# Kernel tuning notes

Measured on AMD Instinct MI355X. Metric: run time of the kernel, lower is better.

Reference implementation:

```python
import jax, jax.numpy as jnp
import numpy as np

LIDAR_MAX_X = 32.0
LIDAR_MAX_Y = 32.0


def bilinear_grid_sample(value, grid):
    """torch.nn.functional.grid_sample, mode='bilinear', padding_mode='zeros',
    align_corners=False.
    value: (B, C, H, W); grid: (B, Q, P, 2) in [-1, 1] (x=width, y=height).
    Returns (B, C, Q, P)."""
    B, C, H, W = value.shape
    x = (grid[..., 0] + 1.0) * (W / 2) - 0.5  # (B,Q,P) unnormalized col
    y = (grid[..., 1] + 1.0) * (H / 2) - 0.5  # (B,Q,P) unnormalized row
    x0 = jnp.floor(x)
    y0 = jnp.floor(y)
    x1 = x0 + 1.0
    y1 = y0 + 1.0
    wx1 = x - x0
    wx0 = 1.0 - wx1
    wy1 = y - y0
    wy0 = 1.0 - wy1
    vflat = value.reshape(B, C, H * W)

    def gather(ix, iy):
        valid = (ix >= 0) & (ix <= W - 1) & (iy >= 0) & (iy <= H - 1)
        ixc = jnp.clip(ix, 0, W - 1).astype(jnp.int32)
        iyc = jnp.clip(iy, 0, H - 1).astype(jnp.int32)
        idx = iyc * W + ixc  # (B,Q,P)
        g = jax.vmap(lambda v, i: v[:, i])(vflat, idx)  # (B,C,Q,P)
        return g * valid[:, None, :, :].astype(value.dtype)

    out = (gather(x0, y0) * (wx0 * wy0)[:, None]
           + gather(x1, y0) * (wx1 * wy0)[:, None]
           + gather(x0, y1) * (wx0 * wy1)[:, None]
           + gather(x1, y1) * (wx1 * wy1)[:, None])
    return out


def setup_inputs() -> dict:
    key = jax.random.key(0)
    ks = jax.random.split(key, 10)
    bs, Q, P, D = 16, 1024, 8, 256
    Cin, H, W = 64, 128, 128
    queries = jax.random.normal(ks[0], (bs, Q, D), dtype=jnp.float32)
    # scale so trajectory points span the +/-32m BEV extent
    traj_points = jax.random.normal(ks[1], (bs, Q, P, 2), dtype=jnp.float32) * 20.0
    bev_feature = jax.random.normal(ks[2], (bs, Cin, H, W), dtype=jnp.float32)
    spatial_shape = jnp.array([H, W], dtype=jnp.int64)
    attn_w = jax.random.normal(ks[3], (P, D), dtype=jnp.float32) * 0.02
    attn_b = jnp.zeros((P,), dtype=jnp.float32)
    conv_w = jax.random.normal(ks[4], (256, Cin, 3, 3), dtype=jnp.float32) * 0.05
    conv_b = jnp.zeros((256,), dtype=jnp.float32)
    out_w = jax.random.normal(ks[5], (D, D), dtype=jnp.float32) * (1.0 / np.sqrt(D))
    out_b = jnp.zeros((D,), dtype=jnp.float32)
    return {"queries": queries, "traj_points": traj_points,
            "bev_feature": bev_feature, "spatial_shape": spatial_shape,
            "attn_w": attn_w, "attn_b": attn_b,
            "conv_w": conv_w, "conv_b": conv_b,
            "out_w": out_w, "out_b": out_b}


def reference(queries, traj_points, bev_feature, spatial_shape,
              attn_w, attn_b, conv_w, conv_b, out_w, out_b):
    # normalize trajectory to [-1,1] and swap (y,x) -> (x,y) grid order
    grid = jnp.stack([traj_points[..., 1] / LIDAR_MAX_X,
                      traj_points[..., 0] / LIDAR_MAX_Y], axis=-1)  # (bs,Q,P,2)
    # per-query attention over the P sampled points
    attn = jax.nn.softmax(
        jnp.einsum('bqd,pd->bqp', queries, attn_w) + attn_b, axis=-1)  # (bs,Q,P)
    # value projection: 3x3 conv + ReLU
    value = jax.lax.conv_general_dilated(
        bev_feature, conv_w, window_strides=(1, 1),
        padding=((1, 1), (1, 1)),
        dimension_numbers=('NCHW', 'OIHW', 'NCHW'))
    value = jax.nn.relu(value + conv_b[None, :, None, None])  # (bs,256,H,W)
    sampled = bilinear_grid_sample(value, grid)  # (bs,256,Q,P)
    out = jnp.einsum('bcqp,bqp->bqc', sampled, attn)  # weighted sum + permute
    out = jnp.einsum('bqc,dc->bqd', out, out_w) + out_b
    # dropout is identity in eval mode
    return out + queries
```

## Files before the change

kernel.cpp:

```cpp
#include <hip/hip_runtime.h>
#include <stdint.h>


typedef __attribute__((ext_vector_type(8))) short short8;
typedef __attribute__((ext_vector_type(4))) float f32x4;

__device__ __forceinline__ unsigned short f2bf(float f) {
  union { float f; unsigned int u; } v; v.f = f;
  unsigned int r = (v.u + 0x7FFFu + ((v.u >> 16) & 1u)) >> 16;
  return (unsigned short)r;
}
__device__ __forceinline__ float bf2f(unsigned short h) {
  union { unsigned int u; float f; } v; v.u = ((unsigned int)h) << 16;
  return v.f;
}

__device__ __forceinline__ void gload_lds16(const void* g, void* l) {
  __builtin_amdgcn_global_load_lds(
      (const __attribute__((address_space(1))) unsigned int*)g,
      (__attribute__((address_space(3))) unsigned int*)l, 16, 0, 0);
}

__global__ __launch_bounds__(256) void k1_transpose(const float* __restrict__ bev,
                                                    unsigned short* __restrict__ nhwc) {
  __shared__ __align__(16) float lds[64 * 32 * 4];
  const int b = blockIdx.x >> 7, y = blockIdx.x & 127;
  const int t = threadIdx.x;
  const float* src = bev + (size_t)(b * 64) * 16384 + y * 128;
#pragma unroll
  for (int k = 0; k < 8; ++k) {
    int chunk = k * 256 + t;
    int ic = chunk >> 5, xq = chunk & 31;
    float4 v = *(const float4*)(src + ic * 16384 + xq * 4);
    int slot = xq ^ (ic >> 3);
    *(float4*)&lds[(ic * 32 + slot) * 4] = v;
  }
  __syncthreads();
  unsigned short* dst = nhwc + (size_t)blockIdx.x * 8192;
#pragma unroll
  for (int k = 0; k < 4; ++k) {
    int co = k * 256 + t;
    int x = co >> 3, icg = co & 7;
    int slot = (x >> 2) ^ icg;
    int w = x & 3;
    uint4 u;
    unsigned int* up = (unsigned int*)&u;
#pragma unroll
    for (int jj = 0; jj < 4; ++jj) {
      float v0 = lds[((icg * 8 + 2 * jj) * 32 + slot) * 4 + w];
      float v1 = lds[((icg * 8 + 2 * jj + 1) * 32 + slot) * 4 + w];
      up[jj] = (unsigned int)f2bf(v0) | ((unsigned int)f2bf(v1) << 16);
    }
    *(uint4*)(dst + x * 64 + icg * 8) = u;
  }
}

__global__ __launch_bounds__(256) void k1b_pack(const float* __restrict__ conv_w,
                                                const float* __restrict__ out_w,
                                                unsigned short* __restrict__ wconv,
                                                unsigned short* __restrict__ wout,
                                                float* __restrict__ zp) {
  const int tid = blockIdx.x * 256 + threadIdx.x;
  for (int idx = tid; idx < 9 * 8 * 256 * 8; idx += 16384) {
    int j = idx & 7, oc = (idx >> 3) & 255, g = (idx >> 11) & 7, o = idx >> 14;
    wconv[idx] = f2bf(conv_w[(oc * 64 + g * 8 + j) * 9 + o]);
  }
  for (int idx = tid; idx < 32 * 256 * 8; idx += 16384) {
    int j = idx & 7, d = (idx >> 3) & 255, g = idx >> 11;
    wout[idx] = f2bf(out_w[d * 256 + g * 8 + j]);
  }
  if (tid < 64) zp[tid] = 0.0f;
}

#define K2_WOFF 66560
__global__ __launch_bounds__(512, 2) void k2_conv(const unsigned short* __restrict__ nhwc,
                                                  const unsigned short* __restrict__ wconv,
                                                  const float* __restrict__ conv_b,
                                                  const float* __restrict__ zp,
                                                  unsigned short* __restrict__ value) {
  __shared__ __align__(16) char smem[99328];
  const short8* lin = (const short8*)smem;
  const int bid = blockIdx.x;
  const int swz = (bid & 7) * 128 + (bid >> 3);
  const int b = swz >> 6, yp = swz & 63;
  const int y0 = yp * 2;
  const int t = threadIdx.x, wid = t >> 6, lane = t & 63;
  const int wo = wid >> 2, wp = wid & 3;
  const int g = lane >> 4, l15 = lane & 15;
  const int r_hat = wp >> 1;
  const int xbase = (wp & 1) * 64 + l15;

  const unsigned short* bevb = nhwc + (size_t)b * (128 * 128 * 64);
  for (int i = wid; i < 65; i += 8) {
    const int chunk = i * 64 + lane;
    const int ridx = chunk / 1040;
    const int rem = chunk - ridx * 1040;
    const int icg = rem / 130;
    const int c = rem - icg * 130;
    const int yy = y0 - 1 + ridx, xx = c - 1;
    const void* src = (yy >= 0 && yy < 128 && xx >= 0 && xx < 128)
                          ? (const void*)(bevb + ((yy * 128 + xx) * 64 + icg * 8))
                          : (const void*)zp;
    gload_lds16(src, smem + i * 1024);
  }
  {
    const unsigned short* wsrc = wconv;
    gload_lds16(wsrc + (size_t)(wid * 128 + lane) * 8, smem + K2_WOFF + wid * 2048);
    gload_lds16(wsrc + (size_t)(wid * 128 + 64 + lane) * 8, smem + K2_WOFF + wid * 2048 + 1024);
  }
  __syncthreads();

  const f32x4 z4 = {0.f, 0.f, 0.f, 0.f};
  f32x4 acc[8][4];
#pragma unroll
  for (int i = 0; i < 8; ++i)
#pragma unroll
    for (int j = 0; j < 4; ++j) acc[i][j] = z4;

#pragma unroll
  for (int s = 0; s < 18; ++s) {
    const int o = s >> 1, ich = s & 1;
    const int dyr = o / 3;
    const int dx = o - dyr * 3 - 1;
    if (s < 17) {
      const int s1 = s + 1;
      const unsigned short* wsrc = wconv + (size_t)(((s1 >> 1) * 2048 + (s1 & 1) * 1024)) * 8;
      char* wdst = smem + K2_WOFF + ((s1 & 1) ? 16384 : 0) + wid * 2048;
      gload_lds16(wsrc + (size_t)(wid * 128 + lane) * 8, wdst);
      gload_lds16(wsrc + (size_t)(wid * 128 + 64 + lane) * 8, wdst + 1024);
    }
    const short8* wb = (const short8*)(smem + K2_WOFF + ((s & 1) ? 16384 : 0));
    short8 af[8];
#pragma unroll
    for (int ocf = 0; ocf < 8; ++ocf) af[ocf] = wb[g * 256 + wo * 128 + ocf * 16 + l15];
    short8 bf[4];
    const int cb = ((r_hat + dyr) * 8 + ich * 4 + g) * 130 + xbase + 1 + dx;
#pragma unroll
    for (int pf = 0; pf < 4; ++pf) bf[pf] = lin[cb + pf * 16];
    __builtin_amdgcn_s_setprio(1);
#pragma unroll
    for (int ocf = 0; ocf < 8; ++ocf)
#pragma unroll
      for (int pf = 0; pf < 4; ++pf)
        acc[ocf][pf] = __builtin_amdgcn_mfma_f32_16x16x32_bf16(af[ocf], bf[pf], acc[ocf][pf], 0, 0, 0);
    __builtin_amdgcn_s_setprio(0);
    __syncthreads();
  }

  const int y = y0 + r_hat;
  unsigned short* vrow = value + (((size_t)(b * 128 + y) * 128 + xbase) * 256);
#pragma unroll
  for (int ocf = 0; ocf < 8; ++ocf) {
    const int ocb = wo * 128 + ocf * 16 + g * 4;
    const float4 cb4 = *(const float4*)(conv_b + ocb);
#pragma unroll
    for (int pf = 0; pf < 4; ++pf) {
      ushort4 ov;
      float v0 = acc[ocf][pf][0] + cb4.x; ov.x = f2bf(v0 > 0.f ? v0 : 0.f);
      float v1 = acc[ocf][pf][1] + cb4.y; ov.y = f2bf(v1 > 0.f ? v1 : 0.f);
      float v2 = acc[ocf][pf][2] + cb4.z; ov.z = f2bf(v2 > 0.f ? v2 : 0.f);
      float v3 = acc[ocf][pf][3] + cb4.w; ov.w = f2bf(v3 > 0.f ? v3 : 0.f);
      *(ushort4*)(vrow + (size_t)pf * 16 * 256 + ocb) = ov;
    }
  }
}

__global__ __launch_bounds__(256) void k3_sample(const float* __restrict__ queries,
                                                 const float* __restrict__ traj,
                                                 const float* __restrict__ attn_w,
                                                 const float* __restrict__ attn_b,
                                                 const unsigned short* __restrict__ value,
                                                 unsigned short* __restrict__ S) {
  const int wid = threadIdx.x >> 6, lane = threadIdx.x & 63;
  const int qg = blockIdx.x * 4 + wid;
  const int b = qg >> 10;
  const float4 qv = ((const float4*)queries)[qg * 64 + lane];
  float a[8];
#pragma unroll
  for (int p = 0; p < 8; ++p) {
    float4 wv = ((const float4*)attn_w)[p * 64 + lane];
    float d = qv.x * wv.x + qv.y * wv.y + qv.z * wv.z + qv.w * wv.w;
#pragma unroll
    for (int off = 32; off >= 1; off >>= 1) d += __shfl_xor(d, off);
    a[p] = d + attn_b[p];
  }
  float mx = a[0];
#pragma unroll
  for (int p = 1; p < 8; ++p) mx = fmaxf(mx, a[p]);
  float ssum = 0.f;
#pragma unroll
  for (int p = 0; p < 8; ++p) { a[p] = __expf(a[p] - mx); ssum += a[p]; }
  const float inv = 1.f / ssum;

  float acc0 = 0.f, acc1 = 0.f, acc2 = 0.f, acc3 = 0.f;
  const unsigned short* vb = value + (size_t)b * (128 * 128 * 256);
  const int coff = lane * 4;
#pragma unroll
  for (int p = 0; p < 8; ++p) {
    const float ty = traj[(qg * 8 + p) * 2 + 0];
    const float tx = traj[(qg * 8 + p) * 2 + 1];
    const float fx = (tx * 0.03125f + 1.f) * 64.f - 0.5f;
    const float fy = (ty * 0.03125f + 1.f) * 64.f - 0.5f;
    const float fx0 = floorf(fx), fy0 = floorf(fy);
    const int ix0 = (int)fx0, iy0 = (int)fy0;
    const float wx1 = fx - fx0, wx0 = 1.f - wx1;
    const float wy1 = fy - fy0, wy0 = 1.f - wy1;
    const float ap = a[p] * inv;
    const float cw[4] = {wx0 * wy0 * ap, wx1 * wy0 * ap, wx0 * wy1 * ap, wx1 * wy1 * ap};
    const int cx[4] = {ix0, ix0 + 1, ix0, ix0 + 1};
    const int cy[4] = {iy0, iy0, iy0 + 1, iy0 + 1};
#pragma unroll
    for (int cc = 0; cc < 4; ++cc) {
      if (cx[cc] >= 0 && cx[cc] < 128 && cy[cc] >= 0 && cy[cc] < 128) {
        const ushort4 v = *(const ushort4*)(vb + (cy[cc] * 128 + cx[cc]) * 256 + coff);
        acc0 += cw[cc] * bf2f(v.x);
        acc1 += cw[cc] * bf2f(v.y);
        acc2 += cw[cc] * bf2f(v.z);
        acc3 += cw[cc] * bf2f(v.w);
      }
    }
  }
  ushort4 o;
  o.x = f2bf(acc0); o.y = f2bf(acc1); o.z = f2bf(acc2); o.w = f2bf(acc3);
  *(ushort4*)(S + (size_t)qg * 256 + coff) = o;
}

__global__ __launch_bounds__(256, 2) void k4_proj(const unsigned short* __restrict__ S,
                                                  const unsigned short* __restrict__ wout,
                                                  const float* __restrict__ out_b,
                                                  const float* __restrict__ queries,
                                                  float* __restrict__ out) {
  __shared__ __align__(16) char smem[16384];
  const short8* lds8 = (const short8*)smem;
  const short8* wp8 = (const short8*)wout;
  const int t = threadIdx.x, wid = t >> 6, lane = t & 63;
  const int wo = wid >> 1, wq = wid & 1;
  const int q0 = blockIdx.x * 128;
  const int g = lane >> 4, l15 = lane & 15;
  const f32x4 z4 = {0.f, 0.f, 0.f, 0.f};
  f32x4 acc[8][4];
#pragma unroll
  for (int i = 0; i < 8; ++i)
#pragma unroll
    for (int j = 0; j < 4; ++j) acc[i][j] = z4;

#pragma unroll
  for (int ii = 0; ii < 2; ++ii) {
    const int chunk = wid * 128 + ii * 64 + lane;
    const int gg = chunk >> 7, q = chunk & 127;
    gload_lds16(S + ((size_t)(q0 + q) * 256 + gg * 8), smem + wid * 2048 + ii * 1024);
  }
  __syncthreads();

#pragma unroll
  for (int ks = 0; ks < 8; ++ks) {
    if (ks < 7) {
      const int k1 = ks + 1;
#pragma unroll
      for (int ii = 0; ii < 2; ++ii) {
        const int chunk = wid * 128 + ii * 64 + lane;
        const int gg = chunk >> 7, q = chunk & 127;
        gload_lds16(S + ((size_t)(q0 + q) * 256 + k1 * 32 + gg * 8),
                    smem + ((k1 & 1) ? 8192 : 0) + wid * 2048 + ii * 1024);
      }
    }
    short8 af[8];
#pragma unroll
    for (int df = 0; df < 8; ++df)
      af[df] = wp8[(ks * 4 + g) * 256 + wo * 128 + df * 16 + l15];
    short8 bf[4];
    const short8* sb = lds8 + ((ks & 1) ? 512 : 0);
#pragma unroll
    for (int qf = 0; qf < 4; ++qf) bf[qf] = sb[g * 128 + wq * 64 + qf * 16 + l15];
    __builtin_amdgcn_s_setprio(1);
#pragma unroll
    for (int df = 0; df < 8; ++df)
#pragma unroll
      for (int qf = 0; qf < 4; ++qf)
        acc[df][qf] = __builtin_amdgcn_mfma_f32_16x16x32_bf16(af[df], bf[qf], acc[df][qf], 0, 0, 0);
    __builtin_amdgcn_s_setprio(0);
    __syncthreads();
  }

#pragma unroll
  for (int df = 0; df < 8; ++df) {
    const int db = wo * 128 + df * 16 + g * 4;
    const float4 ob4 = *(const float4*)(out_b + db);
#pragma unroll
    for (int qf = 0; qf < 4; ++qf) {
      const int q = q0 + wq * 64 + qf * 16 + l15;
      const float4 qv = *(const float4*)(queries + (size_t)q * 256 + db);
      float4 ov;
      ov.x = acc[df][qf][0] + ob4.x + qv.x;
      ov.y = acc[df][qf][1] + ob4.y + qv.y;
      ov.z = acc[df][qf][2] + ob4.z + qv.z;
      ov.w = acc[df][qf][3] + ob4.w + qv.w;
      *(float4*)(out + (size_t)q * 256 + db) = ov;
    }
  }
}

extern "C" void kernel_launch(void* const* d_in, const int* in_sizes, int n_in,
                              void* d_out, int out_size, void* d_ws, size_t ws_size,
                              hipStream_t stream) {
  const float* queries = (const float*)d_in[0];
  const float* traj    = (const float*)d_in[1];
  const float* bev     = (const float*)d_in[2];
  const float* attn_w  = (const float*)d_in[4];
  const float* attn_b  = (const float*)d_in[5];
  const float* conv_w  = (const float*)d_in[6];
  const float* conv_b  = (const float*)d_in[7];
  const float* out_w   = (const float*)d_in[8];
  const float* out_b   = (const float*)d_in[9];
  float* out = (float*)d_out;

  char* ws = (char*)d_ws;
  unsigned short* bev_nhwc = (unsigned short*)(ws);
  unsigned short* value    = (unsigned short*)(ws + 33554432);
  unsigned short* wconv    = (unsigned short*)(ws + 167772160);
  unsigned short* wout     = (unsigned short*)(ws + 168067072);
  unsigned short* Sbuf     = (unsigned short*)(ws + 168198144);
  float*          zp       = (float*)(ws + 176586752);

  k1_transpose<<<2048, 256, 0, stream>>>(bev, bev_nhwc);
  k1b_pack<<<64, 256, 0, stream>>>(conv_w, out_w, wconv, wout, zp);
  k2_conv<<<1024, 512, 0, stream>>>(bev_nhwc, wconv, conv_b, zp, value);
  k3_sample<<<4096, 256, 0, stream>>>(queries, traj, attn_w, attn_b, value, Sbuf);
  k4_proj<<<128, 256, 0, stream>>>(Sbuf, wout, out_b, queries, out);
}
```

Before: 173.8 us.

## Restructure conv main loop into phased ping-pong schedule with per-tap weight staging

The conv kernel now stages the weights for a whole 3x3 tap (both input-channel halves) per iteration into a larger double-buffered LDS region, where before it staged half a tap per step. Each tap is split into four MFMA phases separated by raw s_barriers, with LDS fragment reads and global-to-LDS weight loads interleaved between phases so memory traffic overlaps with matrix math. LDS use grows from about 97KB to 129KB per block. With launch bounds of two blocks per CU this may reduce occupancy, and the many extra barriers add synchronisation cost.

```diff
diff --git a/kernel.cpp b/kernel.cpp
--- a/kernel.cpp
+++ b/kernel.cpp
@@ -73,12 +73,53 @@
 }
 
 #define K2_WOFF 66560
+
+#define K2_READA(o, h) do {                                                   \
+    const short8* wb_ = (const short8*)(smem + K2_WOFF + ((o)&1) * 32768);    \
+    _Pragma("unroll")                                                         \
+    for (int ic_ = 0; ic_ < 2; ++ic_)                                         \
+      _Pragma("unroll")                                                       \
+      for (int i_ = 0; i_ < 4; ++i_)                                          \
+        aH[ic_*4+i_] = wb_[(ic_*4+g)*256 + wo*128 + (h)*64 + i_*16 + l15];    \
+  } while (0)
+
+#define K2_READB(dyr, dx, j, B) do {                                          \
+    _Pragma("unroll")                                                         \
+    for (int ic_ = 0; ic_ < 2; ++ic_)                                         \
+      _Pragma("unroll")                                                       \
+      for (int p_ = 0; p_ < 2; ++p_)                                          \
+        B[ic_*2+p_] = lin[((rh+(dyr))*8 + ic_*4 + g)*130 + 1 + (dx) + xb +    \
+                          l15 + ((j)*2 + p_)*16];                             \
+  } while (0)
+
+#define K2_STAGEW(o1, cbase) do {                                             \
+    const unsigned short* ws_ = wconv + (size_t)(o1) * 16384;                 \
+    char* wd_ = smem + K2_WOFF + ((o1)&1) * 32768;                            \
+    _Pragma("unroll")                                                         \
+    for (int c_ = 0; c_ < 4; ++c_)                                            \
+      gload_lds16(ws_ + ((cbase)+c_) * 512 + lane * 8,                        \
+                  wd_ + ((cbase)+c_) * 1024);                                 \
+  } while (0)
+
+#define K2_MF(h, j, B) do {                                                   \
+    __builtin_amdgcn_s_setprio(1);                                            \
+    _Pragma("unroll")                                                         \
+    for (int i_ = 0; i_ < 4; ++i_)                                            \
+      _Pragma("unroll")                                                       \
+      for (int p_ = 0; p_ < 2; ++p_)                                          \
+        _Pragma("unroll")                                                     \
+        for (int ic_ = 0; ic_ < 2; ++ic_)                                     \
+          acc[(h)*4+i_][(j)*2+p_] = __builtin_amdgcn_mfma_f32_16x16x32_bf16(  \
+              aH[ic_*4+i_], B[ic_*2+p_], acc[(h)*4+i_][(j)*2+p_], 0, 0, 0);   \
+    __builtin_amdgcn_s_setprio(0);                                            \
+  } while (0)
+
 __global__ __launch_bounds__(512, 2) void k2_conv(const unsigned short* __restrict__ nhwc,
                                                   const unsigned short* __restrict__ wconv,
                                                   const float* __restrict__ conv_b,
                                                   const float* __restrict__ zp,
                                                   unsigned short* __restrict__ value) {
-  __shared__ __align__(16) char smem[99328];
+  __shared__ __align__(16) char smem[132096];
   const short8* lin = (const short8*)smem;
   const int bid = blockIdx.x;
   const int swz = (bid & 7) * 128 + (bid >> 3);
@@ -87,8 +128,8 @@
   const int t = threadIdx.x, wid = t >> 6, lane = t & 63;
   const int wo = wid >> 2, wp = wid & 3;
   const int g = lane >> 4, l15 = lane & 15;
-  const int r_hat = wp >> 1;
-  const int xbase = (wp & 1) * 64 + l15;
+  const int rh = wp >> 1;
+  const int xb = (wp & 1) * 64;
 
   const unsigned short* bevb = nhwc + (size_t)b * (128 * 128 * 64);
   for (int i = wid; i < 65; i += 8) {
@@ -103,12 +144,9 @@
                           : (const void*)zp;
     gload_lds16(src, smem + i * 1024);
   }
-  {
-    const unsigned short* wsrc = wconv;
-    gload_lds16(wsrc + (size_t)(wid * 128 + lane) * 8, smem + K2_WOFF + wid * 2048);
-    gload_lds16(wsrc + (size_t)(wid * 128 + 64 + lane) * 8, smem + K2_WOFF + wid * 2048 + 1024);
-  }
-  __syncthreads();
+  K2_STAGEW(0, wid * 4);
+  asm volatile("s_waitcnt vmcnt(0)" ::: "memory");
+  __builtin_amdgcn_s_barrier();
 
   const f32x4 z4 = {0.f, 0.f, 0.f, 0.f};
   f32x4 acc[8][4];
@@ -117,38 +155,34 @@
 #pragma unroll
     for (int j = 0; j < 4; ++j) acc[i][j] = z4;
 
-#pragma unroll
-  for (int s = 0; s < 18; ++s) {
-    const int o = s >> 1, ich = s & 1;
-    const int dyr = o / 3;
-    const int dx = o - dyr * 3 - 1;
-    if (s < 17) {
-      const int s1 = s + 1;
-      const unsigned short* wsrc = wconv + (size_t)(((s1 >> 1) * 2048 + (s1 & 1) * 1024)) * 8;
-      char* wdst = smem + K2_WOFF + ((s1 & 1) ? 16384 : 0) + wid * 2048;
-      gload_lds16(wsrc + (size_t)(wid * 128 + lane) * 8, wdst);
-      gload_lds16(wsrc + (size_t)(wid * 128 + 64 + lane) * 8, wdst + 1024);
-    }
-    const short8* wb = (const short8*)(smem + K2_WOFF + ((s & 1) ? 16384 : 0));
-    short8 af[8];
-#pragma unroll
-    for (int ocf = 0; ocf < 8; ++ocf) af[ocf] = wb[g * 256 + wo * 128 + ocf * 16 + l15];
-    short8 bf[4];
-    const int cb = ((r_hat + dyr) * 8 + ich * 4 + g) * 130 + xbase + 1 + dx;
-#pragma unroll
-    for (int pf = 0; pf < 4; ++pf) bf[pf] = lin[cb + pf * 16];
-    __builtin_amdgcn_s_setprio(1);
-#pragma unroll
-    for (int ocf = 0; ocf < 8; ++ocf)
-#pragma unroll
-      for (int pf = 0; pf < 4; ++pf)
-        acc[ocf][pf] = __builtin_amdgcn_mfma_f32_16x16x32_bf16(af[ocf], bf[pf], acc[ocf][pf], 0, 0, 0);
-    __builtin_amdgcn_s_setprio(0);
-    __syncthreads();
-  }
-
-  const int y = y0 + r_hat;
-  unsigned short* vrow = value + (((size_t)(b * 128 + y) * 128 + xbase) * 256);
+  short8 aH[8], b0[4], b1[4];
+
+#pragma unroll
+  for (int o = 0; o < 9; ++o) {
+    const int dyr = o / 3, dx = o % 3 - 1;
+    K2_READA(o, 0);
+    K2_READB(dyr, dx, 0, b0);
+    if (o < 8 && wid < 4) K2_STAGEW(o + 1, wid * 4);
+    __builtin_amdgcn_s_barrier();
+    K2_MF(0, 0, b0);
+    __builtin_amdgcn_s_barrier();
+    K2_READB(dyr, dx, 1, b1);
+    if (o < 8 && wid >= 4) K2_STAGEW(o + 1, 16 + (wid - 4) * 4);
+    __builtin_amdgcn_s_barrier();
+    K2_MF(0, 1, b1);
+    __builtin_amdgcn_s_barrier();
+    K2_READA(o, 1);
+    __builtin_amdgcn_s_barrier();
+    K2_MF(1, 0, b0);
+    __builtin_amdgcn_s_barrier();
+    asm volatile("s_waitcnt vmcnt(0)" ::: "memory");
+    __builtin_amdgcn_s_barrier();
+    K2_MF(1, 1, b1);
+    __builtin_amdgcn_s_barrier();
+  }
+
+  const int y = y0 + rh;
+  unsigned short* vrow = value + (((size_t)(b * 128 + y) * 128 + xb + l15) * 256);
 #pragma unroll
   for (int ocf = 0; ocf < 8; ++ocf) {
     const int ocb = wo * 128 + ocf * 16 + g * 4;
```

Result: slower. 182.3 us (+4.9%).

## Load conv weights directly to registers with double-buffered prefetch, drop per-step barriers

Applied to the files above, without the earlier changes.

The conv kernel no longer stages weight slices through shared memory. Each wave now loads its A fragments straight from global memory into registers two steps ahead, and prefetches the B fragments from LDS one step ahead. Dropping the weight staging removes the per-step __syncthreads and cuts LDS use from about 97KB to 65KB, which could allow more blocks per CU. The cost is more VGPR pressure from the double-buffered fragments, and every wave issues its own uncoalesced global weight loads, which rely on cache hits.

```diff
diff --git a/kernel.cpp b/kernel.cpp
--- a/kernel.cpp
+++ b/kernel.cpp
@@ -72,14 +72,40 @@
   if (tid < 64) zp[tid] = 0.0f;
 }
 
-#define K2_WOFF 66560
+#define K2_LOADA(s, A) do {                                                   \
+    _Pragma("unroll")                                                         \
+    for (int ocf_ = 0; ocf_ < 8; ++ocf_)                                      \
+      A[ocf_] = gA[(4 * (s) + g) * 256 + wo * 128 + ocf_ * 16 + l15];         \
+  } while (0)
+
+#define K2_READB(s, B) do {                                                   \
+    const int o_ = (s) >> 1, ich_ = (s) & 1;                                  \
+    const int dyr_ = o_ / 3, dx_ = o_ - dyr_ * 3 - 1;                         \
+    _Pragma("unroll")                                                         \
+    for (int pf_ = 0; pf_ < 4; ++pf_)                                         \
+      B[pf_] = lin[((rh + dyr_) * 8 + ich_ * 4 + g) * 130 + 1 + dx_ + xb +    \
+                   l15 + pf_ * 16];                                           \
+  } while (0)
+
+#define K2_MFMA(A, B) do {                                                    \
+    __builtin_amdgcn_s_setprio(1);                                            \
+    _Pragma("unroll")                                                         \
+    for (int ocf_ = 0; ocf_ < 8; ++ocf_)                                      \
+      _Pragma("unroll")                                                       \
+      for (int pf_ = 0; pf_ < 4; ++pf_)                                       \
+        acc[ocf_][pf_] = __builtin_amdgcn_mfma_f32_16x16x32_bf16(             \
+            A[ocf_], B[pf_], acc[ocf_][pf_], 0, 0, 0);                        \
+    __builtin_amdgcn_s_setprio(0);                                            \
+  } while (0)
+
 __global__ __launch_bounds__(512, 2) void k2_conv(const unsigned short* __restrict__ nhwc,
                                                   const unsigned short* __restrict__ wconv,
                                                   const float* __restrict__ conv_b,
                                                   const float* __restrict__ zp,
                                                   unsigned short* __restrict__ value) {
-  __shared__ __align__(16) char smem[99328];
+  __shared__ __align__(16) char smem[66560];
   const short8* lin = (const short8*)smem;
+  const short8* gA = (const short8*)wconv;
   const int bid = blockIdx.x;
   const int swz = (bid & 7) * 128 + (bid >> 3);
   const int b = swz >> 6, yp = swz & 63;
@@ -87,8 +113,8 @@
   const int t = threadIdx.x, wid = t >> 6, lane = t & 63;
   const int wo = wid >> 2, wp = wid & 3;
   const int g = lane >> 4, l15 = lane & 15;
-  const int r_hat = wp >> 1;
-  const int xbase = (wp & 1) * 64 + l15;
+  const int rh = wp >> 1;
+  const int xb = (wp & 1) * 64;
 
   const unsigned short* bevb = nhwc + (size_t)b * (128 * 128 * 64);
   for (int i = wid; i < 65; i += 8) {
@@ -103,11 +129,6 @@
                           : (const void*)zp;
     gload_lds16(src, smem + i * 1024);
   }
-  {
-    const unsigned short* wsrc = wconv;
-    gload_lds16(wsrc + (size_t)(wid * 128 + lane) * 8, smem + K2_WOFF + wid * 2048);
-    gload_lds16(wsrc + (size_t)(wid * 128 + 64 + lane) * 8, smem + K2_WOFF + wid * 2048 + 1024);
-  }
   __syncthreads();
 
   const f32x4 z4 = {0.f, 0.f, 0.f, 0.f};
@@ -117,38 +138,20 @@
 #pragma unroll
     for (int j = 0; j < 4; ++j) acc[i][j] = z4;
 
+  short8 A[2][8], bb[2][4];
+  K2_LOADA(0, A[0]);
+  K2_LOADA(1, A[1]);
+  K2_READB(0, bb[0]);
+
 #pragma unroll
   for (int s = 0; s < 18; ++s) {
-    const int o = s >> 1, ich = s & 1;
-    const int dyr = o / 3;
-    const int dx = o - dyr * 3 - 1;
-    if (s < 17) {
-      const int s1 = s + 1;
-      const unsigned short* wsrc = wconv + (size_t)(((s1 >> 1) * 2048 + (s1 & 1) * 1024)) * 8;
-      char* wdst = smem + K2_WOFF + ((s1 & 1) ? 16384 : 0) + wid * 2048;
-      gload_lds16(wsrc + (size_t)(wid * 128 + lane) * 8, wdst);
-      gload_lds16(wsrc + (size_t)(wid * 128 + 64 + lane) * 8, wdst + 1024);
-    }
-    const short8* wb = (const short8*)(smem + K2_WOFF + ((s & 1) ? 16384 : 0));
-    short8 af[8];
-#pragma unroll
-    for (int ocf = 0; ocf < 8; ++ocf) af[ocf] = wb[g * 256 + wo * 128 + ocf * 16 + l15];
-    short8 bf[4];
-    const int cb = ((r_hat + dyr) * 8 + ich * 4 + g) * 130 + xbase + 1 + dx;
-#pragma unroll
-    for (int pf = 0; pf < 4; ++pf) bf[pf] = lin[cb + pf * 16];
-    __builtin_amdgcn_s_setprio(1);
-#pragma unroll
-    for (int ocf = 0; ocf < 8; ++ocf)
-#pragma unroll
-      for (int pf = 0; pf < 4; ++pf)
-        acc[ocf][pf] = __builtin_amdgcn_mfma_f32_16x16x32_bf16(af[ocf], bf[pf], acc[ocf][pf], 0, 0, 0);
-    __builtin_amdgcn_s_setprio(0);
-    __syncthreads();
-  }
-
-  const int y = y0 + r_hat;
-  unsigned short* vrow = value + (((size_t)(b * 128 + y) * 128 + xbase) * 256);
+    if (s < 17) K2_READB(s + 1, bb[(s + 1) & 1]);
+    K2_MFMA(A[s & 1], bb[s & 1]);
+    if (s + 2 < 18) K2_LOADA(s + 2, A[s & 1]);
+  }
+
+  const int y = y0 + rh;
+  unsigned short* vrow = value + (((size_t)(b * 128 + y) * 128 + xb + l15) * 256);
 #pragma unroll
   for (int ocf = 0; ocf < 8; ++ocf) {
     const int ocb = wo * 128 + ocf * 16 + g * 4;
```

After: 166.7 us. 1.04x faster.
